# Optimization experiments

Hardware: AMD Instinct MI355X
Metric: run time of the kernel (lower is better)

## Reference

```python
import jax, jax.numpy as jnp
import numpy as np

N = 512          # data_info['n']
K = 513          # data_info['k'] + 1
B = 65536        # batch size


def _build_adjust(n, k):
    # Reproduces the __init__ mask construction exactly.
    a1 = np.ones((n - 1, k - 1, 2), dtype=np.float32)
    a2 = np.zeros((n - 1, k - 1, 2), dtype=np.float32)
    for i in range(0, k - 2):
        if i >= n - 1:
            break
        f1 = a1[i].reshape(-1)
        f1[2 + 2 * i:] = 0
        a1[i] = f1.reshape(k - 1, 2)
        f2 = a2[i].reshape(-1)
        f2[2 + 2 * i + 1] = 1
        a2[i] = f2.reshape(k - 1, 2)
    return jnp.asarray(a1), jnp.asarray(a2)


W_ADJ1, W_ADJ2 = _build_adjust(N, K)


def setup_inputs() -> dict:
    key = jax.random.key(0)
    k1, k2, k3 = jax.random.split(key, 3)
    x = jax.random.randint(k1, (B, N), 0, 2, dtype=jnp.int32)
    W = jax.random.normal(k2, (N - 1, K - 1, 2), dtype=jnp.float32)
    endW = jax.random.normal(k3, (1, K), dtype=jnp.float32)
    return {"x": x, "W": W, "endW": endW}


def reference(x, W, endW):
    # W_full construction (softmax over the 2-way split, masked, with the
    # deterministic [1,0] row prepended along the group axis).
    Wsm = jax.nn.softmax(W, axis=2)                      # (n-1, k-1, 2)
    W_full = Wsm * W_ADJ1 + W_ADJ2                       # (n-1, k-1, 2)
    append = jnp.zeros((N - 1, 1, 2), W_full.dtype).at[:, :, 0].set(1.0)
    W_full = jnp.concatenate([append, W_full], axis=1)   # (n-1, k, 2)

    # group_num at step i is the running cumsum of x[:, 0..i]; the serial
    # recurrence collapses to a single cumsum, letting us gather all steps
    # at once instead of the original n-1 step Python loop.
    g = jnp.cumsum(x, axis=1)                            # (B, n)
    steps = jnp.arange(N - 1)                            # step i -> W_full[i-1]
    vals = W_full[steps[None, :], g[:, 1:], x[:, 1:]]    # (B, n-1)
    out = jnp.sum(jnp.log(vals), axis=1, keepdims=True)  # (B, 1)

    e = jax.nn.softmax(endW, axis=1)[0]                  # (k,)
    out = out + jnp.log(e[g[:, -1]])[:, None]            # (B, 1)
    return out
```

## Files before the change

### kernel.cpp

```cpp
#include <hip/hip_runtime.h>
#include <math.h>

#define NN     512
#define KK     513
#define BB     65536
#define TROWS  512
#define TCOLS  513

__global__ void build_table_kernel(const float* __restrict__ W, float* __restrict__ T) {
    int idx = blockIdx.x * blockDim.x + threadIdx.x;
    if (idx >= TROWS * TCOLS) return;
    int t = idx / TCOLS;
    int g = idx - t * TCOLS;
    float v0 = 0.f, v1 = 0.f;
    if (t >= 1 && g >= 1 && g <= t) {
        const float* w = W + ((size_t)(t - 1) * (KK - 1) + (g - 1)) * 2;
        float w0 = w[0], w1 = w[1];
        float m  = fmaxf(w0, w1);
        float lse = m + logf(expf(w0 - m) + expf(w1 - m));
        v0 = w0 - lse;
        v1 = w1 - lse;
    }
    T[2 * idx + 0] = v0;
    T[2 * idx + 1] = v1;
}

__global__ void build_endw_kernel(const float* __restrict__ endW, float* __restrict__ logE) {
    int lane = threadIdx.x;
    float vals[9];
    float m = -1e30f;
    #pragma unroll
    for (int k = 0; k < 9; ++k) {
        int i = lane + 64 * k;
        vals[k] = (i < KK) ? endW[i] : -1e30f;
        m = fmaxf(m, vals[k]);
    }
    #pragma unroll
    for (int d = 32; d >= 1; d >>= 1) m = fmaxf(m, __shfl_xor(m, d, 64));
    float s = 0.f;
    #pragma unroll
    for (int k = 0; k < 9; ++k) s += expf(vals[k] - m);
    #pragma unroll
    for (int d = 32; d >= 1; d >>= 1) s += __shfl_xor(s, d, 64);
    float lse = m + logf(s);
    #pragma unroll
    for (int k = 0; k < 9; ++k) {
        int i = lane + 64 * k;
        if (i < KK) logE[i] = endW[i] - lse;
    }
}

__global__ __launch_bounds__(256) void pc_main_kernel(
    const int* __restrict__ x, const float* __restrict__ T,
    const float* __restrict__ logE, float* __restrict__ out)
{
    const int row = blockIdx.x * blockDim.x + threadIdx.x;
    if (row >= BB) return;
    const int4* xp = (const int4*)(x + (size_t)row * NN);

    float a0 = 0.f, a1 = 0.f, a2 = 0.f, a3 = 0.f;
    int g = 0;

    int4 c0 = xp[0], c1 = xp[1], c2 = xp[2], c3 = xp[3];

    for (int ch = 0; ch < 32; ++ch) {
        int4 n0 = make_int4(0, 0, 0, 0), n1 = n0, n2 = n0, n3 = n0;
        if (ch < 31) {
            const int4* p = xp + (ch + 1) * 4;
            n0 = p[0]; n1 = p[1]; n2 = p[2]; n3 = p[3];
        }
        const int xs[16] = { c0.x, c0.y, c0.z, c0.w,
                             c1.x, c1.y, c1.z, c1.w,
                             c2.x, c2.y, c2.z, c2.w,
                             c3.x, c3.y, c3.z, c3.w };
        const int tb = ch * 16;
        #pragma unroll
        for (int k = 0; k < 16; ++k) {
            g += xs[k];
            const float v = T[((tb + k) * TCOLS + g) * 2 + xs[k]];
            if      ((k & 3) == 0) a0 += v;
            else if ((k & 3) == 1) a1 += v;
            else if ((k & 3) == 2) a2 += v;
            else                   a3 += v;
        }
        c0 = n0; c1 = n1; c2 = n2; c3 = n3;
    }
    out[row] = (a0 + a1) + (a2 + a3) + logE[g];
}

extern "C" void kernel_launch(void* const* d_in, const int* in_sizes, int n_in,
                              void* d_out, int out_size, void* d_ws, size_t ws_size,
                              hipStream_t stream)
{
    const int*   x    = (const int*)d_in[0];
    const float* W    = (const float*)d_in[1];
    const float* endW = (const float*)d_in[2];
    float*       out  = (float*)d_out;

    float* T    = (float*)d_ws;
    float* logE = (float*)((char*)d_ws + (size_t)TROWS * TCOLS * 2 * sizeof(float));

    {
        int total  = TROWS * TCOLS;
        int blocks = (total + 255) / 256;
        build_table_kernel<<<blocks, 256, 0, stream>>>(W, T);
    }
    build_endw_kernel<<<1, 64, 0, stream>>>(endW, logE);
    pc_main_kernel<<<BB / 256, 256, 0, stream>>>(x, T, logE, out);
}
```

Baseline: 208.6 us.

## Deepen x prefetch to two 32-element chunks with nontemporal loads and batched gathers

The main loop now handles 32 elements per chunk, keeps two chunks of x in flight, and fully unrolls the 16 chunks. All 32 table gathers in a chunk are issued before they are accumulated, so more memory-level parallelism hides the latency of the dependent table lookups. x is read with nontemporal loads so the streamed input does not evict the reused table from cache, and the bounds check is removed. The cost is much higher register use, which can lower occupancy.

Result: slower. 243.4 us (+16.7%).

```diff
diff --git a/kernel.cpp b/kernel.cpp
--- a/kernel.cpp
+++ b/kernel.cpp
@@ -6,6 +6,8 @@
 #define BB     65536
 #define TROWS  512
 #define TCOLS  513
+
+typedef int iv4 __attribute__((ext_vector_type(4)));
 
 __global__ void build_table_kernel(const float* __restrict__ W, float* __restrict__ T) {
     int idx = blockIdx.x * blockDim.x + threadIdx.x;
@@ -55,35 +57,47 @@
     const float* __restrict__ logE, float* __restrict__ out)
 {
     const int row = blockIdx.x * blockDim.x + threadIdx.x;
-    if (row >= BB) return;
-    const int4* xp = (const int4*)(x + (size_t)row * NN);
+    const iv4* xp = (const iv4*)(x + (size_t)row * NN);
 
     float a0 = 0.f, a1 = 0.f, a2 = 0.f, a3 = 0.f;
     int g = 0;
 
-    int4 c0 = xp[0], c1 = xp[1], c2 = xp[2], c3 = xp[3];
+    iv4 c[8], n[8];
+    #pragma unroll
+    for (int j = 0; j < 8; ++j) c[j] = __builtin_nontemporal_load(&xp[j]);
+    #pragma unroll
+    for (int j = 0; j < 8; ++j) n[j] = __builtin_nontemporal_load(&xp[8 + j]);
 
-    for (int ch = 0; ch < 32; ++ch) {
-        int4 n0 = make_int4(0, 0, 0, 0), n1 = n0, n2 = n0, n3 = n0;
-        if (ch < 31) {
-            const int4* p = xp + (ch + 1) * 4;
-            n0 = p[0]; n1 = p[1]; n2 = p[2]; n3 = p[3];
+    #pragma unroll
+    for (int ch = 0; ch < 16; ++ch) {
+        int xs[32];
+        #pragma unroll
+        for (int j = 0; j < 8; ++j) {
+            xs[4 * j + 0] = c[j].x;
+            xs[4 * j + 1] = c[j].y;
+            xs[4 * j + 2] = c[j].z;
+            xs[4 * j + 3] = c[j].w;
         }
-        const int xs[16] = { c0.x, c0.y, c0.z, c0.w,
-                             c1.x, c1.y, c1.z, c1.w,
-                             c2.x, c2.y, c2.z, c2.w,
-                             c3.x, c3.y, c3.z, c3.w };
-        const int tb = ch * 16;
+        float v[32];
         #pragma unroll
-        for (int k = 0; k < 16; ++k) {
+        for (int k = 0; k < 32; ++k) {
             g += xs[k];
-            const float v = T[((tb + k) * TCOLS + g) * 2 + xs[k]];
-            if      ((k & 3) == 0) a0 += v;
-            else if ((k & 3) == 1) a1 += v;
-            else if ((k & 3) == 2) a2 += v;
-            else                   a3 += v;
+            v[k] = T[(ch * 32 + k) * (2 * TCOLS) + 2 * g + xs[k]];
         }
-        c0 = n0; c1 = n1; c2 = n2; c3 = n3;
+        #pragma unroll
+        for (int j = 0; j < 8; ++j) c[j] = n[j];
+        if (ch < 14) {
+            const iv4* p = xp + (ch + 2) * 8;
+            #pragma unroll
+            for (int j = 0; j < 8; ++j) n[j] = __builtin_nontemporal_load(&p[j]);
+        }
+        #pragma unroll
+        for (int k = 0; k < 32; ++k) {
+            if      ((k & 3) == 0) a0 += v[k];
+            else if ((k & 3) == 1) a1 += v[k];
+            else if ((k & 3) == 2) a2 += v[k];
+            else                   a3 += v[k];
+        }
     }
     out[row] = (a0 + a1) + (a2 + a3) + logE[g];
 }
```
